# Optimization experiments

Measured on AMD Instinct MI355X. Metric: run time of the kernel, lower is better.

The kernel has to match this reference:

```python
import jax, jax.numpy as jnp
import numpy as np
from jax import lax

T, B, D = 2048, 16, 1024


def setup_inputs() -> dict:
    key = jax.random.key(0)
    ks = jax.random.split(key, 3)
    xavier = (6.0 / (D + D)) ** 0.5  # xavier_uniform bound
    x = jax.random.normal(ks[0], (T, B, D), dtype=jnp.float32)
    W_alpha = jax.random.uniform(ks[1], (D, D), jnp.float32, -xavier, xavier)
    W_x = jax.random.uniform(ks[2], (D, D), jnp.float32, -xavier, xavier)
    b_alpha = jnp.full((D,), 2.0, jnp.float32)  # init_alpha_bias
    d_g = jnp.full((D,), 0.5, jnp.float32)      # init_d_g
    b_g = jnp.full((D,), 0.5, jnp.float32)      # init_b_g
    b_v = jnp.zeros((D,), jnp.float32)
    return {"x": x, "W_alpha": W_alpha, "b_alpha": b_alpha, "d_g": d_g,
            "b_g": b_g, "W_x": W_x, "b_v": b_v}


def reference(x, W_alpha, b_alpha, d_g, b_g, W_x, b_v):
    Tn, Bn, Dn = x.shape
    # Batched input projections (as in the torch code, done before the loop)
    alpha_all = jax.nn.sigmoid(jnp.einsum('tbd,ed->tbe', x, W_alpha) + b_alpha)  # [T,B,D]
    v_raw_all = jnp.tanh(jnp.einsum('tbd,ed->tbe', x, W_x) + b_v)                # [T,B,D]

    h0 = jnp.zeros((Bn, Dn), x.dtype)

    def step(h_prev, inp):
        alpha, v_raw = inp
        g = jax.nn.sigmoid(-d_g * jnp.abs(h_prev) + b_g)  # inverse self-gating
        v = v_raw * g
        h_new = alpha * h_prev + (1.0 - alpha) * v
        out = h_new * jax.nn.silu(h_new)
        return h_new, (h_new, out)

    _, (hs, outs) = lax.scan(step, h0, (alpha_all, v_raw_all))
    h = jnp.concatenate([h0[None], hs], axis=0)  # [T+1,B,D]
    return outs, h
```

## Files before the change

kernel.cpp:

```cpp
#include <hip/hip_runtime.h>
#include <hip/hip_fp16.h>

#define T_DIM 2048
#define B_DIM 16
#define D_DIM 1024
#define M_TOT (T_DIM * B_DIM)
#define N_TOT (2 * D_DIM)
#define K_TOT D_DIM
#define BD    (B_DIM * D_DIM)

typedef __attribute__((ext_vector_type(8))) short short8;
typedef __attribute__((ext_vector_type(4))) float floatx4;

__device__ __forceinline__ short f32_to_bf16(float f) {
  unsigned u = __float_as_uint(f);
  u = (u + 0x7FFFu + ((u >> 16) & 1u)) >> 16;
  return (short)u;
}

__global__ __launch_bounds__(256) void cast_bf16_k(const float* __restrict__ src,
                                                   short* __restrict__ dst) {
  const size_t i = ((size_t)blockIdx.x * 256 + threadIdx.x) * 8;
  floatx4 f0 = *(const floatx4*)(src + i);
  floatx4 f1 = *(const floatx4*)(src + i + 4);
  short8 o;
  o[0] = f32_to_bf16(f0[0]); o[1] = f32_to_bf16(f0[1]);
  o[2] = f32_to_bf16(f0[2]); o[3] = f32_to_bf16(f0[3]);
  o[4] = f32_to_bf16(f1[0]); o[5] = f32_to_bf16(f1[1]);
  o[6] = f32_to_bf16(f1[2]); o[7] = f32_to_bf16(f1[3]);
  *(short8*)(dst + i) = o;
}

#define GLDS16(gp, lp)                                                                   \
  __builtin_amdgcn_global_load_lds((const __attribute__((address_space(1))) void*)(gp),  \
                                   (__attribute__((address_space(3))) void*)(lp), 16, 0, 0)

__global__ __launch_bounds__(256, 2) void gemm_act_k(
    const short* __restrict__ xb, const short* __restrict__ wb,
    const float* __restrict__ b_alpha, const float* __restrict__ b_v,
    __half* __restrict__ pairbuf) {
  __shared__ __align__(16) short As[128 * 32];
  __shared__ __align__(16) short Bs[128 * 32];
  const int tid  = threadIdx.x;
  const int wave = tid >> 6;
  const int lane = tid & 63;
  const int quad = lane >> 4;
  const int l16  = lane & 15;
  const int mblk = blockIdx.y << 7;
  const int nblk = blockIdx.x << 7;
  const int wrow = (wave >> 1) << 6;
  const int wcol = (wave & 1) << 6;

  floatx4 acc[4][4];
#pragma unroll
  for (int i = 0; i < 4; ++i)
#pragma unroll
    for (int j = 0; j < 4; ++j) acc[i][j] = {0.f, 0.f, 0.f, 0.f};

  const int chunk_m = tid >> 2;
  const int chunk_c = tid & 3;
  const short* gA0 = xb + (size_t)(mblk + chunk_m) * K_TOT + chunk_c * 8;
  const short* gA1 = gA0 + (size_t)64 * K_TOT;
  const short* gB0 = wb + (size_t)(nblk + chunk_m) * K_TOT + chunk_c * 8;
  const short* gB1 = gB0 + (size_t)64 * K_TOT;
  short* lA0 = As + wave * 512;
  short* lA1 = As + 2048 + wave * 512;
  short* lB0 = Bs + wave * 512;
  short* lB1 = Bs + 2048 + wave * 512;

  const int aoff = (wrow + l16) * 32 + quad * 8;
  const int boff = (wcol + l16) * 32 + quad * 8;

  for (int k0 = 0; k0 < K_TOT; k0 += 32) {
    GLDS16(gA0 + k0, lA0);
    GLDS16(gA1 + k0, lA1);
    GLDS16(gB0 + k0, lB0);
    GLDS16(gB1 + k0, lB1);
    __syncthreads();
    short8 af[4], bf[4];
#pragma unroll
    for (int i = 0; i < 4; ++i) af[i] = *(const short8*)(As + aoff + i * 512);
#pragma unroll
    for (int i = 0; i < 4; ++i) bf[i] = *(const short8*)(Bs + boff + i * 512);
#pragma unroll
    for (int i = 0; i < 4; ++i)
#pragma unroll
      for (int j = 0; j < 4; ++j)
        acc[i][j] = __builtin_amdgcn_mfma_f32_16x16x32_bf16(af[i], bf[j], acc[i][j], 0, 0, 0);
    __syncthreads();
  }

  const bool isA = (nblk < D_DIM);
  const float* __restrict__ bias = isA ? b_alpha : b_v;
  const int hsel = isA ? 0 : 1;
#pragma unroll
  for (int j = 0; j < 4; ++j) {
    const int n_g = nblk + wcol + j * 16 + l16;
    const int e = isA ? n_g : (n_g - D_DIM);
    const float bz = bias[e];
#pragma unroll
    for (int i = 0; i < 4; ++i) {
      const floatx4 v = acc[i][j];
      const int m_base = mblk + wrow + i * 16 + quad * 4;
#pragma unroll
      for (int r = 0; r < 4; ++r) {
        const float z = v[r] + bz;
        float val;
        if (isA) {
          val = __builtin_amdgcn_rcpf(1.f + __expf(-z));
        } else {
          val = 1.f - 2.f * __builtin_amdgcn_rcpf(__expf(2.f * z) + 1.f);
        }
        pairbuf[((size_t)(m_base + r) * D_DIM + e) * 2 + hsel] = __float2half(val);
      }
    }
  }
}

__global__ __launch_bounds__(64) void scan_k(const __half2* __restrict__ pair,
                                             const float* __restrict__ d_g,
                                             const float* __restrict__ b_g,
                                             float* __restrict__ outbuf) {
  const int c = blockIdx.x * 64 + threadIdx.x;
  const float LOG2E = 1.44269504f;
  const float dg = d_g[c & (D_DIM - 1)] * LOG2E;
  const float bg = b_g[c & (D_DIM - 1)] * LOG2E;
  float* __restrict__ outs = outbuf;
  float* __restrict__ hout = outbuf + (size_t)T_DIM * BD;
  hout[c] = 0.f;
  float h = 0.f;
  size_t idx = c;
  __half2 p[8];
#pragma unroll
  for (int k = 0; k < 8; ++k) p[k] = pair[idx + (size_t)k * BD];
  for (int t = 0; t < T_DIM; t += 8) {
    const size_t pfadd = (t + 8 < T_DIM) ? (size_t)8 * BD : 0;
#pragma unroll
    for (int k = 0; k < 8; ++k) {
      const float2 av = __half22float2(p[k]);
      p[k] = pair[idx + pfadd];
      const float w = (1.f - av.x) * av.y;
      const float e = __builtin_amdgcn_exp2f(fmaf(dg, fabsf(h), -bg));
      const float g = __builtin_amdgcn_rcpf(1.f + e);
      h = fmaf(av.x, h, w * g);
      const float s = __builtin_amdgcn_rcpf(1.f + __builtin_amdgcn_exp2f(-LOG2E * h));
      outs[idx] = h * h * s;
      hout[idx + BD] = h;
      idx += BD;
    }
  }
}

extern "C" void kernel_launch(void* const* d_in, const int* in_sizes, int n_in,
                              void* d_out, int out_size, void* d_ws, size_t ws_size,
                              hipStream_t stream) {
  const float* x       = (const float*)d_in[0];
  const float* W_alpha = (const float*)d_in[1];
  const float* b_alpha = (const float*)d_in[2];
  const float* d_g     = (const float*)d_in[3];
  const float* b_g     = (const float*)d_in[4];
  const float* W_x     = (const float*)d_in[5];
  const float* b_v     = (const float*)d_in[6];
  float* out = (float*)d_out;

  char* ws = (char*)d_ws;
  short*  xb      = (short*)ws;
  short*  wb      = (short*)(ws + (size_t)67108864);
  __half* pairbuf = (__half*)(ws + (size_t)71303168);

  cast_bf16_k<<<M_TOT * K_TOT / (8 * 256), 256, 0, stream>>>(x, xb);
  cast_bf16_k<<<D_DIM * K_TOT / (8 * 256), 256, 0, stream>>>(W_alpha, wb);
  cast_bf16_k<<<D_DIM * K_TOT / (8 * 256), 256, 0, stream>>>(W_x, wb + (size_t)D_DIM * K_TOT);
  gemm_act_k<<<dim3(N_TOT / 128, M_TOT / 128), 256, 0, stream>>>(xb, wb, b_alpha, b_v, pairbuf);
  scan_k<<<BD / 64, 64, 0, stream>>>((const __half2*)pairbuf, d_g, b_g, out);
}
```

Before: 691.1 us.

## Split scan output into fp16 h stream plus parallel silu expansion kernel; swizzle GEMM LDS

The serial scan now writes only an fp16 hidden state per step, and a new fully parallel kernel expands it into the fp32 h and output tensors. This takes the large fp32 stores off the latency-bound recurrence. The GEMM's LDS layout is XOR-swizzled to reduce bank conflicts, and the scan prefetch depth is doubled. Storing h in fp16 lowers output precision and adds an extra pass over memory.

```diff
diff --git a/kernel.cpp b/kernel.cpp
--- a/kernel.cpp
+++ b/kernel.cpp
@@ -58,18 +58,19 @@
     for (int j = 0; j < 4; ++j) acc[i][j] = {0.f, 0.f, 0.f, 0.f};
 
   const int chunk_m = tid >> 2;
-  const int chunk_c = tid & 3;
-  const short* gA0 = xb + (size_t)(mblk + chunk_m) * K_TOT + chunk_c * 8;
+  const int c_swz   = (tid & 3) ^ (chunk_m & 3) ^ ((chunk_m >> 2) & 1);
+  const short* gA0 = xb + (size_t)(mblk + chunk_m) * K_TOT + c_swz * 8;
   const short* gA1 = gA0 + (size_t)64 * K_TOT;
-  const short* gB0 = wb + (size_t)(nblk + chunk_m) * K_TOT + chunk_c * 8;
+  const short* gB0 = wb + (size_t)(nblk + chunk_m) * K_TOT + c_swz * 8;
   const short* gB1 = gB0 + (size_t)64 * K_TOT;
   short* lA0 = As + wave * 512;
   short* lA1 = As + 2048 + wave * 512;
   short* lB0 = Bs + wave * 512;
   short* lB1 = Bs + 2048 + wave * 512;
 
-  const int aoff = (wrow + l16) * 32 + quad * 8;
-  const int boff = (wcol + l16) * 32 + quad * 8;
+  const int pl   = (l16 & 3) ^ ((l16 >> 2) & 1);
+  const int aoff = (wrow + l16) * 32 + ((quad ^ pl) * 8);
+  const int boff = (wcol + l16) * 32 + ((quad ^ pl) * 8);
 
   for (int k0 = 0; k0 < K_TOT; k0 += 32) {
     GLDS16(gA0 + k0, lA0);
@@ -120,34 +121,57 @@
 __global__ __launch_bounds__(64) void scan_k(const __half2* __restrict__ pair,
                                              const float* __restrict__ d_g,
                                              const float* __restrict__ b_g,
-                                             float* __restrict__ outbuf) {
+                                             __half* __restrict__ hh) {
   const int c = blockIdx.x * 64 + threadIdx.x;
   const float LOG2E = 1.44269504f;
   const float dg = d_g[c & (D_DIM - 1)] * LOG2E;
   const float bg = b_g[c & (D_DIM - 1)] * LOG2E;
-  float* __restrict__ outs = outbuf;
-  float* __restrict__ hout = outbuf + (size_t)T_DIM * BD;
-  hout[c] = 0.f;
+  hh[c] = __float2half(0.f);
   float h = 0.f;
   size_t idx = c;
-  __half2 p[8];
-#pragma unroll
-  for (int k = 0; k < 8; ++k) p[k] = pair[idx + (size_t)k * BD];
-  for (int t = 0; t < T_DIM; t += 8) {
-    const size_t pfadd = (t + 8 < T_DIM) ? (size_t)8 * BD : 0;
-#pragma unroll
-    for (int k = 0; k < 8; ++k) {
+  __half2 p[16];
+#pragma unroll
+  for (int k = 0; k < 16; ++k) p[k] = pair[idx + (size_t)k * BD];
+  for (int t = 0; t < T_DIM; t += 16) {
+    const size_t pfadd = (t + 16 < T_DIM) ? (size_t)16 * BD : 0;
+#pragma unroll
+    for (int k = 0; k < 16; ++k) {
       const float2 av = __half22float2(p[k]);
       p[k] = pair[idx + pfadd];
       const float w = (1.f - av.x) * av.y;
       const float e = __builtin_amdgcn_exp2f(fmaf(dg, fabsf(h), -bg));
       const float g = __builtin_amdgcn_rcpf(1.f + e);
       h = fmaf(av.x, h, w * g);
-      const float s = __builtin_amdgcn_rcpf(1.f + __builtin_amdgcn_exp2f(-LOG2E * h));
-      outs[idx] = h * h * s;
-      hout[idx + BD] = h;
+      hh[idx + BD] = __float2half(h);
       idx += BD;
     }
+  }
+}
+
+__global__ __launch_bounds__(256) void silu_k(const __half* __restrict__ hh,
+                                              float* __restrict__ outbuf) {
+  const float LOG2E = 1.44269504f;
+  const size_t i = ((size_t)blockIdx.x * 256 + threadIdx.x) * 8;
+  float* __restrict__ outs = outbuf;
+  float* __restrict__ hout = outbuf + (size_t)T_DIM * BD;
+  const __half2* hp = (const __half2*)(hh + i);
+  float hf[8];
+#pragma unroll
+  for (int j = 0; j < 4; ++j) {
+    const float2 f = __half22float2(hp[j]);
+    hf[2 * j] = f.x; hf[2 * j + 1] = f.y;
+  }
+  *(floatx4*)(hout + i)     = floatx4{hf[0], hf[1], hf[2], hf[3]};
+  *(floatx4*)(hout + i + 4) = floatx4{hf[4], hf[5], hf[6], hf[7]};
+  if (i >= BD) {
+    float o[8];
+#pragma unroll
+    for (int j = 0; j < 8; ++j) {
+      const float s = __builtin_amdgcn_rcpf(1.f + __builtin_amdgcn_exp2f(-LOG2E * hf[j]));
+      o[j] = hf[j] * hf[j] * s;
+    }
+    *(floatx4*)(outs + i - BD)     = floatx4{o[0], o[1], o[2], o[3]};
+    *(floatx4*)(outs + i - BD + 4) = floatx4{o[4], o[5], o[6], o[7]};
   }
 }
 
@@ -167,10 +191,12 @@
   short*  xb      = (short*)ws;
   short*  wb      = (short*)(ws + (size_t)67108864);
   __half* pairbuf = (__half*)(ws + (size_t)71303168);
+  __half* h_half  = (__half*)ws;
 
   cast_bf16_k<<<M_TOT * K_TOT / (8 * 256), 256, 0, stream>>>(x, xb);
   cast_bf16_k<<<D_DIM * K_TOT / (8 * 256), 256, 0, stream>>>(W_alpha, wb);
   cast_bf16_k<<<D_DIM * K_TOT / (8 * 256), 256, 0, stream>>>(W_x, wb + (size_t)D_DIM * K_TOT);
   gemm_act_k<<<dim3(N_TOT / 128, M_TOT / 128), 256, 0, stream>>>(xb, wb, b_alpha, b_v, pairbuf);
-  scan_k<<<BD / 64, 64, 0, stream>>>((const __half2*)pairbuf, d_g, b_g, out);
-}
+  scan_k<<<BD / 64, 64, 0, stream>>>((const __half2*)pairbuf, d_g, b_g, h_half);
+  silu_k<<<(T_DIM + 1) * BD / (8 * 256), 256, 0, stream>>>(h_half, out);
+}
```

After: 673.8 us. -2.5%, faster.
